# Kernel optimization log

Measured on AMD Instinct MI355X. Metric: run time of the kernel, lower is better.

Reference implementation:

```python
import jax, jax.numpy as jnp
import numpy as np

SHIFTS = [1, 2, 4]  # matches init_kwargs 'shifts' (all in range 0 < s < channels)


def setup_inputs() -> dict:
    key = jax.random.key(0)
    k1, k2, k3 = jax.random.split(key, 3)
    B, H, L, D = 4, 1, 2048, 512
    factor = 4
    proj_in = 2 * len(SHIFTS) * D  # cli_mode='full' -> 2 components per shift
    x = jax.random.normal(k1, (B, H, L, D), dtype=jnp.float32)
    W = jax.random.normal(k2, (factor, D), dtype=jnp.float32) * 0.05
    # glorot-ish scale for the projection kernel
    proj_kernel = jax.random.normal(k3, (proj_in, D), dtype=jnp.float32) * (1.0 / np.sqrt(proj_in))
    proj_bias = jnp.zeros((D,), dtype=jnp.float32)
    return {"x": x, "W": W, "proj_kernel": proj_kernel, "proj_bias": proj_bias}


def reference(x, W, proj_kernel, proj_bias):
    # x: (B, H, L, D); W: (k, D) slot multivectors
    k, D = W.shape
    B, H, L, _ = x.shape
    # coarse[-1] treated as zeros; non-anchor slots source previous coarse vector
    coarse_prev = jnp.pad(x, ((0, 0), (0, 0), (1, 0), (0, 0)))[:, :, :-1, :]
    # src: (B, H, L, k, D) — slots 0..k-2 from coarse_prev, slot k-1 (anchor) from x
    src = jnp.concatenate(
        [jnp.repeat(coarse_prev[:, :, :, None, :], k - 1, axis=3),
         x[:, :, :, None, :]],
        axis=3,
    )
    W_b = W[None, None, None, :, :]  # (1,1,1,k,D)
    components = []
    for s in SHIFTS:
        src_s = jnp.roll(src, s, axis=-1)
        W_s_b = jnp.roll(W, s, axis=-1)[None, None, None, :, :]
        sw = src * W_s_b
        components.append(sw - W_b * src_s)        # wedge part
        components.append(jax.nn.silu(sw))          # inner part (full mode)
    g = jnp.concatenate(components, axis=-1)  # (B,H,L,k, 2*len(shifts)*D)
    fine = jnp.einsum('bhlkc,cd->bhlkd', g, proj_kernel) + proj_bias
    return fine.reshape(B, H, L * k, D)
```

## Files before the change

### kernel.cpp

```cpp
#include <hip/hip_runtime.h>
#include <cstdint>
#include <cstddef>

#define D_DIM 512
#define L_DIM 2048
#define KB_DIM 2048
#define KS_DIM 1536
#define NROWS_X 2049
#define M_TOT 32768

typedef __bf16 bf16x8 __attribute__((ext_vector_type(8)));
typedef float  f32x4  __attribute__((ext_vector_type(4)));

__device__ __forceinline__ unsigned f2bf(float f) {
  unsigned u = __float_as_uint(f);
  u += 0x7FFF + ((u >> 16) & 1);
  return u >> 16;
}
__device__ __forceinline__ float bf2f(unsigned short u) {
  return __uint_as_float(((unsigned)u) << 16);
}
__device__ __forceinline__ void gld_lds16(const void* g, void* l) {
  __builtin_amdgcn_global_load_lds((const __attribute__((address_space(1))) void*)g,
                                   (__attribute__((address_space(3))) void*)l,
                                   16, 0, 0);
}

__global__ void convert_x(const float* __restrict__ x, unsigned short* __restrict__ XbfZ) {
  const int b = blockIdx.y;
  const int idx = blockIdx.x * 256 + threadIdx.x;
  if (idx >= NROWS_X * 128) return;
  const int rr = idx >> 7;
  const int c4 = idx & 127;
  uint2 p = {0u, 0u};
  if (rr > 0) {
    float4 v = reinterpret_cast<const float4*>(x)[((size_t)b * L_DIM + rr - 1) * 128 + c4];
    p.x = f2bf(v.x) | (f2bf(v.y) << 16);
    p.y = f2bf(v.z) | (f2bf(v.w) << 16);
  }
  reinterpret_cast<uint2*>(XbfZ)[((size_t)b * NROWS_X + rr) * 128 + c4] = p;
}

__global__ void build_B(const float* __restrict__ P, const float* __restrict__ W,
                        unsigned short* __restrict__ Ball,
                        unsigned short* __restrict__ Wtab, int buildWtab) {
  if (buildWtab && blockIdx.x == 0) {
    for (int i = threadIdx.x; i < 6144; i += 256) {
      const int c = i & 511; const int rest = i >> 9;
      const int si = rest % 3; const int jj = rest / 3;
      Wtab[(jj * 3 + si) * 512 + c] =
          (unsigned short)f2bf(W[jj * 512 + ((c - (1 << si)) & 511)]);
    }
  }
  const int bx = blockIdx.x;
  const int j = bx >> 6, dt = (bx >> 3) & 7, ct = bx & 7;
  const int t = threadIdx.x;
  const int d = dt * 64 + (t & 63);
  const int cbase = ct * 64 + (t >> 6) * 16;
  unsigned short bufd[16];
  unsigned short bufs[3][16];
  #pragma unroll
  for (int cc = 0; cc < 16; ++cc) {
    const int c = cbase + cc;
    float qd = 0.f;
    #pragma unroll
    for (int si = 0; si < 3; ++si) {
      const int s = 1 << si;
      const int cm = (c - s) & 511, cp = (c + s) & 511;
      qd += W[j * 512 + cm] * P[((size_t)(2 * si) * 512 + c) * 512 + d]
          - W[j * 512 + cp] * P[((size_t)(2 * si) * 512 + cp) * 512 + d];
      bufs[si][cc] = (unsigned short)f2bf(P[((size_t)(2 * si + 1) * 512 + c) * 512 + d]);
    }
    bufd[cc] = (unsigned short)f2bf(qd);
  }
  unsigned short* row = Ball + (size_t)(j * 512 + d) * KB_DIM;
  *reinterpret_cast<uint4*>(&row[cbase])     = *reinterpret_cast<uint4*>(&bufd[0]);
  *reinterpret_cast<uint4*>(&row[cbase + 8]) = *reinterpret_cast<uint4*>(&bufd[8]);
  #pragma unroll
  for (int si = 0; si < 3; ++si) {
    *reinterpret_cast<uint4*>(&row[512 + si * 512 + cbase])     = *reinterpret_cast<uint4*>(&bufs[si][0]);
    *reinterpret_cast<uint4*>(&row[512 + si * 512 + cbase + 8]) = *reinterpret_cast<uint4*>(&bufs[si][8]);
  }
}

__global__ void gs_gen(const unsigned short* __restrict__ XbfZ,
                       const unsigned short* __restrict__ Wtab,
                       unsigned short* __restrict__ GS) {
  const int m0 = blockIdx.x * 4;
  const int j = m0 >> 13, b = (m0 >> 11) & 3, lbase = m0 & 2047;
  const int r = threadIdx.x >> 6, lane = threadIdx.x & 63;
  const int l = lbase + r;
  const size_t vrow = (size_t)b * NROWS_X + l + (j == 3);
  union U { uint4 q; unsigned short s[8]; };
  U va;
  va.q = *reinterpret_cast<const uint4*>(XbfZ + vrow * 512 + lane * 8);
  unsigned short* o = GS + (size_t)(m0 + r) * KS_DIM + lane * 8;
  #pragma unroll
  for (int si = 0; si < 3; ++si) {
    U wa;
    wa.q = *reinterpret_cast<const uint4*>(Wtab + (j * 3 + si) * 512 + lane * 8);
    unsigned res[4];
    #pragma unroll
    for (int e = 0; e < 4; ++e) {
      float s0 = bf2f(va.s[2 * e])     * bf2f(wa.s[2 * e]);
      float s1 = bf2f(va.s[2 * e + 1]) * bf2f(wa.s[2 * e + 1]);
      float g0 = s0 * __builtin_amdgcn_rcpf(1.f + __expf(-s0));
      float g1 = s1 * __builtin_amdgcn_rcpf(1.f + __expf(-s1));
      res[e] = f2bf(g0) | (f2bf(g1) << 16);
    }
    uint4 ov = {res[0], res[1], res[2], res[3]};
    *reinterpret_cast<uint4*>(o + si * 512) = ov;
  }
}

#define BARR asm volatile("s_barrier" ::: "memory")
#define VMW(N) asm volatile("s_waitcnt vmcnt(" #N ")" ::: "memory")

#define READ_A(MH, BUF) do { \
  _Pragma("unroll") \
  for (int mf = 0; mf < 4; ++mf) { \
    a[mf][0] = __builtin_bit_cast(bf16x8, *reinterpret_cast<const uint4*>(&A_lds[BUF][aRow[mf] + (MH)*4096 + p0])); \
    a[mf][1] = __builtin_bit_cast(bf16x8, *reinterpret_cast<const uint4*>(&A_lds[BUF][aRow[mf] + (MH)*4096 + p1])); \
  } } while (0)

#define READ_B(NH, BUF, BB) do { \
  _Pragma("unroll") \
  for (int nf = 0; nf < 2; ++nf) { \
    BB[nf][0] = __builtin_bit_cast(bf16x8, *reinterpret_cast<const uint4*>(&B_lds[BUF][bRow[nf] + (NH)*2048 + p0])); \
    BB[nf][1] = __builtin_bit_cast(bf16x8, *reinterpret_cast<const uint4*>(&B_lds[BUF][bRow[nf] + (NH)*2048 + p1])); \
  } } while (0)

#define MFMA_Q(MH, NH, BB) do { \
  _Pragma("unroll") \
  for (int mf = 0; mf < 4; ++mf) { \
    _Pragma("unroll") \
    for (int nf = 0; nf < 2; ++nf) { \
      acc[(MH)*4+mf][(NH)*2+nf] = __builtin_amdgcn_mfma_f32_16x16x32_bf16(a[mf][0], BB[nf][0], acc[(MH)*4+mf][(NH)*2+nf], 0, 0, 0); \
      acc[(MH)*4+mf][(NH)*2+nf] = __builtin_amdgcn_mfma_f32_16x16x32_bf16(a[mf][1], BB[nf][1], acc[(MH)*4+mf][(NH)*2+nf], 0, 0, 0); \
    } } } while (0)

__global__ __launch_bounds__(512, 2) void gemm8(
    const unsigned short* __restrict__ XbfZ, const unsigned short* __restrict__ GS,
    const unsigned short* __restrict__ Ball, const float* __restrict__ bias,
    float* __restrict__ out) {
  __shared__ alignas(16) unsigned short A_lds[2][16384];
  __shared__ alignas(16) unsigned short B_lds[2][16384];

  const int tid = threadIdx.x;
  const int bid = blockIdx.x;
  const int wid = (bid & 7) * 32 + (bid >> 3);
  const int mtile = wid >> 1;
  const int ntile = wid & 1;
  const int j  = mtile >> 5;
  const int b  = (mtile >> 3) & 3;
  const int l0 = (mtile & 7) * 256;
  const int n0 = ntile * 256;
  const size_t mbase = (size_t)((j * 4 + b) * L_DIM + l0);

  const int srow = tid >> 3;
  const int c8   = (tid & 7) ^ (srow & 7);
  const unsigned short* pXd = XbfZ + ((size_t)(b * NROWS_X + (j == 3) + l0 + srow)) * 512 + c8 * 8;
  const unsigned short* pGS = GS + (mbase + srow) * (size_t)KS_DIM + c8 * 8;
  const unsigned short* pB  = Ball + ((size_t)(j * 512 + n0 + srow)) * KB_DIM + c8 * 8;
  const int ldsSlot = tid * 8;

  auto stageA = [&](int TT, int h, int bufi) {
    unsigned short* dst = &A_lds[bufi][h * 8192 + ldsSlot];
    if (TT < 8) {
      const unsigned short* s = pXd + (size_t)h * 128 * 512 + TT * 64;
      gld_lds16(s, dst);
      gld_lds16(s + 64 * 512, dst + 4096);
    } else {
      const unsigned short* s = pGS + (size_t)h * 128 * KS_DIM + (TT - 8) * 64;
      gld_lds16(s, dst);
      gld_lds16(s + 64 * KS_DIM, dst + 4096);
    }
  };
  auto stageB = [&](int TT, int h, int bufi) {
    const unsigned short* s = pB + (size_t)h * 128 * KB_DIM + TT * 64;
    unsigned short* dst = &B_lds[bufi][h * 8192 + ldsSlot];
    gld_lds16(s, dst);
    gld_lds16(s + 64 * KB_DIM, dst + 4096);
  };

  const int lane = tid & 63, wv = tid >> 6;
  const int wm = wv >> 2, wn = wv & 3;
  const int l16 = lane & 15, quad = lane >> 4;
  const int p0 = ((quad)     ^ (l16 & 7)) * 8;
  const int p1 = ((quad + 4) ^ (l16 & 7)) * 8;
  int aRow[4], bRow[2];
  #pragma unroll
  for (int mf = 0; mf < 4; ++mf) aRow[mf] = (wm * 128 + mf * 16 + l16) * 64;
  #pragma unroll
  for (int nf = 0; nf < 2; ++nf) bRow[nf] = (wn * 64 + nf * 16 + l16) * 64;

  f32x4 acc[8][4];
  #pragma unroll
  for (int i = 0; i < 8; ++i)
    #pragma unroll
    for (int n = 0; n < 4; ++n)
      acc[i][n] = f32x4{0.f, 0.f, 0.f, 0.f};

  bf16x8 a[4][2], b0[2][2], b1[2][2];

  stageB(0, 0, 0); stageB(0, 1, 0);
  stageA(0, 0, 0); stageA(0, 1, 0);
  stageB(1, 0, 1); stageB(1, 1, 1);
  VMW(4);
  BARR;

  for (int T = 0; T < 32; ++T) {
    const int cur = T & 1, nxt = cur ^ 1;
    READ_A(0, cur);
    READ_B(0, cur, b0);
    if (T + 1 < 32) stageA(T + 1, 0, nxt);
    BARR;
    __builtin_amdgcn_s_setprio(1);
    MFMA_Q(0, 0, b0);
    __builtin_amdgcn_s_setprio(0);
    BARR;
    READ_B(1, cur, b1);
    if (T + 1 < 32) stageA(T + 1, 1, nxt);
    BARR;
    __builtin_amdgcn_s_setprio(1);
    MFMA_Q(0, 1, b1);
    __builtin_amdgcn_s_setprio(0);
    BARR;
    READ_A(1, cur);
    if (T + 2 < 32) stageB(T + 2, 0, cur);
    BARR;
    __builtin_amdgcn_s_setprio(1);
    MFMA_Q(1, 1, b1);
    __builtin_amdgcn_s_setprio(0);
    BARR;
    if (T + 2 < 32) stageB(T + 2, 1, cur);
    BARR;
    __builtin_amdgcn_s_setprio(1);
    MFMA_Q(1, 0, b0);
    __builtin_amdgcn_s_setprio(0);
    if (T < 30) {
      VMW(4);
      BARR;
    } else if (T == 30) {
      VMW(0);
      BARR;
    }
  }

  #pragma unroll
  for (int nfg = 0; nfg < 4; ++nfg) {
    const int d = n0 + wn * 64 + nfg * 16 + l16;
    const float bv = bias[d];
    #pragma unroll
    for (int mfg = 0; mfg < 8; ++mfg) {
      const int lrow = l0 + wm * 128 + mfg * 16 + quad * 4;
      #pragma unroll
      for (int rg = 0; rg < 4; ++rg) {
        out[((size_t)(b * L_DIM + lrow + rg) * 4 + j) * D_DIM + d] = acc[mfg][nfg][rg] + bv;
      }
    }
  }
}

__global__ __launch_bounds__(256, 2) void fused_gemm(
    const unsigned short* __restrict__ XbfZ, const unsigned short* __restrict__ Ball,
    const float* __restrict__ W, const float* __restrict__ bias,
    float* __restrict__ out) {
  __shared__ alignas(16) unsigned short Vt[2][4096];
  __shared__ alignas(16) unsigned short Bt[2][8192];
  __shared__ alignas(16) unsigned short At[128 * 40];
  __shared__ alignas(16) unsigned short Wr[3 * 512];

  const int tid = threadIdx.x;
  const int nt = blockIdx.x & 1;
  const int mt = blockIdx.x >> 1;
  const int j  = mt >> 6;
  const int b  = (mt >> 4) & 3;
  const int lt = mt & 15;
  const int l0 = lt * 128;
  const int n0 = nt * 256;
  const int base_l = l0 - ((j == 3) ? 0 : 1);

  #pragma unroll
  for (int i = 0; i < 6; ++i) {
    const int idx = tid + i * 256;
    const int si = idx >> 9, c = idx & 511, s = 1 << si;
    Wr[idx] = (unsigned short)f2bf(W[j * 512 + ((c - s) & 511)]);
  }

  const int lane = tid & 63, wv = tid >> 6;
  const int qv = (lane & 3) ^ ((lane >> 4) & 3);
  const int rsub = lane >> 2;
  const unsigned short* gA0 = XbfZ + ((size_t)(b * NROWS_X + 1 + base_l + (wv * 2) * 16 + rsub)) * 512 + qv * 8;
  const unsigned short* gA1 = gA0 + (size_t)16 * 512;
  const unsigned short* gB[4];
  #pragma unroll
  for (int pi = 0; pi < 4; ++pi)
    gB[pi] = Ball + (size_t)(j * 512 + n0 + (wv * 4 + pi) * 16 + rsub) * KB_DIM + qv * 8;
  const int vOff0 = wv * 1024 + lane * 8;
  const int bOff0 = wv * 2048 + lane * 8;

  const int am = tid >> 1;
  const int akh = (tid & 1) * 16;
  const int ch0 = (tid & 1) * 2;
  const int sswz = (am >> 2) & 3;
  unsigned short* aDst = &At[am * 40 + akh];

  const int l16 = lane & 15, quad = lane >> 4;
  const int wm = wv >> 1, wn = wv & 1;
  const int fsw = (l16 >> 2) & 3;
  const int aVoff = (wm * 64 + l16) * 32 + ((quad ^ fsw)) * 8;
  const int aSoff = (wm * 64 + l16) * 40 + quad * 8;
  const int bOffF = (wn * 128 + l16) * 32 + ((quad ^ fsw)) * 8;

  f32x4 acc[4][8];
  #pragma unroll
  for (int i = 0; i < 4; ++i)
    #pragma unroll
    for (int n = 0; n < 8; ++n)
      acc[i][n] = f32x4{0.f, 0.f, 0.f, 0.f};

  {
    gld_lds16(gA0, &Vt[0][vOff0]);
    gld_lds16(gA1, &Vt[0][vOff0 + 512]);
    #pragma unroll
    for (int pi = 0; pi < 4; ++pi)
      gld_lds16(gB[pi], &Bt[0][bOff0 + pi * 512]);
  }

  for (int it = 0; it < 64; ++it) {
    const int buf = it & 1;
    const int kk0 = it * 32;
    const int gi = kk0 >> 9;

    __syncthreads();

    if (it + 1 < 64) {
      const int nk = kk0 + 32;
      const int nv = nk & 511;
      gld_lds16(gA0 + nv, &Vt[buf ^ 1][vOff0]);
      gld_lds16(gA1 + nv, &Vt[buf ^ 1][vOff0 + 512]);
      #pragma unroll
      for (int pi = 0; pi < 4; ++pi)
        gld_lds16(gB[pi] + nk, &Bt[buf ^ 1][bOff0 + pi * 512]);
    }

    bf16x8 af[4], bfr[8];
    if (gi == 0) {
      #pragma unroll
      for (int mi = 0; mi < 4; ++mi) {
        uint4 r = *reinterpret_cast<const uint4*>(&Vt[buf][aVoff + mi * 512]);
        af[mi] = __builtin_bit_cast(bf16x8, r);
      }
    } else {
      const int si = gi - 1;
      const int ccbase = (kk0 & 511) + akh;
      uint4 v0 = *reinterpret_cast<const uint4*>(&Vt[buf][(am * 4 + ((ch0)     ^ sswz)) * 8]);
      uint4 v1 = *reinterpret_cast<const uint4*>(&Vt[buf][(am * 4 + ((ch0 + 1) ^ sswz)) * 8]);
      uint4 w0 = *reinterpret_cast<const uint4*>(&Wr[si * 512 + ccbase]);
      uint4 w1 = *reinterpret_cast<const uint4*>(&Wr[si * 512 + ccbase + 8]);
      union U { uint4 q[2]; unsigned short s[16]; };
      U va, wa; va.q[0] = v0; va.q[1] = v1; wa.q[0] = w0; wa.q[1] = w1;
      unsigned res[8];
      #pragma unroll
      for (int e = 0; e < 8; ++e) {
        float s0 = bf2f(va.s[2 * e])     * bf2f(wa.s[2 * e]);
        float s1 = bf2f(va.s[2 * e + 1]) * bf2f(wa.s[2 * e + 1]);
        float g0 = s0 * __builtin_amdgcn_rcpf(1.f + __expf(-s0));
        float g1 = s1 * __builtin_amdgcn_rcpf(1.f + __expf(-s1));
        res[e] = f2bf(g0) | (f2bf(g1) << 16);
      }
      uint4 o0 = {res[0], res[1], res[2], res[3]};
      uint4 o1 = {res[4], res[5], res[6], res[7]};
      *reinterpret_cast<uint4*>(aDst) = o0;
      *reinterpret_cast<uint4*>(aDst + 8) = o1;
      __syncthreads();
      #pragma unroll
      for (int mi = 0; mi < 4; ++mi) {
        uint4 r = *reinterpret_cast<const uint4*>(&At[aSoff + mi * 640]);
        af[mi] = __builtin_bit_cast(bf16x8, r);
      }
    }
    #pragma unroll
    for (int ni = 0; ni < 8; ++ni) {
      uint4 r = *reinterpret_cast<const uint4*>(&Bt[buf][bOffF + ni * 512]);
      bfr[ni] = __builtin_bit_cast(bf16x8, r);
    }
    #pragma unroll
    for (int mi = 0; mi < 4; ++mi)
      #pragma unroll
      for (int ni = 0; ni < 8; ++ni)
        acc[mi][ni] = __builtin_amdgcn_mfma_f32_16x16x32_bf16(af[mi], bfr[ni], acc[mi][ni], 0, 0, 0);
  }

  #pragma unroll
  for (int ni = 0; ni < 8; ++ni) {
    const int d = n0 + wn * 128 + ni * 16 + l16;
    const float bv = bias[d];
    #pragma unroll
    for (int mi = 0; mi < 4; ++mi) {
      const int lrow = l0 + wm * 64 + mi * 16 + quad * 4;
      #pragma unroll
      for (int rg = 0; rg < 4; ++rg) {
        out[((size_t)(b * L_DIM + lrow + rg) * 4 + j) * D_DIM + d] = acc[mi][ni][rg] + bv;
      }
    }
  }
}

extern "C" void kernel_launch(void* const* d_in, const int* in_sizes, int n_in,
                              void* d_out, int out_size, void* d_ws, size_t ws_size,
                              hipStream_t stream) {
  const float* x    = (const float*)d_in[0];
  const float* W    = (const float*)d_in[1];
  const float* P    = (const float*)d_in[2];
  const float* bias = (const float*)d_in[3];
  float* out = (float*)d_out;

  unsigned short* XbfZ = (unsigned short*)d_ws;
  unsigned short* Ball = XbfZ + (size_t)4 * NROWS_X * 512;
  unsigned short* Wtab = Ball + (size_t)4 * 512 * KB_DIM;
  unsigned short* GS   = Wtab + 6144;
  const size_t need_bytes =
      ((size_t)4 * NROWS_X * 512 + (size_t)4 * 512 * KB_DIM + 6144 +
       (size_t)M_TOT * KS_DIM) * 2;
  const bool primary = ws_size >= need_bytes;

  convert_x<<<dim3(1025, 4), 256, 0, stream>>>(x, XbfZ);
  build_B<<<256, 256, 0, stream>>>(P, W, Ball, Wtab, primary ? 1 : 0);
  if (primary) {
    gs_gen<<<8192, 256, 0, stream>>>(XbfZ, Wtab, GS);
    gemm8<<<dim3(256), dim3(512), 0, stream>>>(XbfZ, GS, Ball, bias, out);
  } else {
    fused_gemm<<<512, 256, 0, stream>>>(XbfZ, Ball, W, bias, out);
  }
}
```

Measured before the change: 184.1 us.

## Switch main GEMM to 32x32x16 MFMA with two-phase K-step schedule

Replaces the 16x16x32 bf16 MFMA tiles in the primary GEMM with 32x32x16 MFMA tiles and 16-wide accumulators. Each K-step is restructured from four barrier-separated quarters into two halves, and both A halves are staged up front. The aim is fewer LDS fragment reads per FLOP, fewer barriers, and higher MFMA throughput per instruction. Risks include higher register pressure from the larger fragment arrays at 2 waves/SIMD, and a changed LDS read/write overlap that could race on buffer reuse.

```diff
diff --git a/kernel.cpp b/kernel.cpp
--- a/kernel.cpp
+++ b/kernel.cpp
@@ -11,6 +11,7 @@
 
 typedef __bf16 bf16x8 __attribute__((ext_vector_type(8)));
 typedef float  f32x4  __attribute__((ext_vector_type(4)));
+typedef float  f32x16 __attribute__((ext_vector_type(16)));
 
 __device__ __forceinline__ unsigned f2bf(float f) {
   unsigned u = __float_as_uint(f);
@@ -115,31 +116,9 @@
 
 #define BARR asm volatile("s_barrier" ::: "memory")
 #define VMW(N) asm volatile("s_waitcnt vmcnt(" #N ")" ::: "memory")
-
-#define READ_A(MH, BUF) do { \
-  _Pragma("unroll") \
-  for (int mf = 0; mf < 4; ++mf) { \
-    a[mf][0] = __builtin_bit_cast(bf16x8, *reinterpret_cast<const uint4*>(&A_lds[BUF][aRow[mf] + (MH)*4096 + p0])); \
-    a[mf][1] = __builtin_bit_cast(bf16x8, *reinterpret_cast<const uint4*>(&A_lds[BUF][aRow[mf] + (MH)*4096 + p1])); \
-  } } while (0)
-
-#define READ_B(NH, BUF, BB) do { \
-  _Pragma("unroll") \
-  for (int nf = 0; nf < 2; ++nf) { \
-    BB[nf][0] = __builtin_bit_cast(bf16x8, *reinterpret_cast<const uint4*>(&B_lds[BUF][bRow[nf] + (NH)*2048 + p0])); \
-    BB[nf][1] = __builtin_bit_cast(bf16x8, *reinterpret_cast<const uint4*>(&B_lds[BUF][bRow[nf] + (NH)*2048 + p1])); \
-  } } while (0)
-
-#define MFMA_Q(MH, NH, BB) do { \
-  _Pragma("unroll") \
-  for (int mf = 0; mf < 4; ++mf) { \
-    _Pragma("unroll") \
-    for (int nf = 0; nf < 2; ++nf) { \
-      acc[(MH)*4+mf][(NH)*2+nf] = __builtin_amdgcn_mfma_f32_16x16x32_bf16(a[mf][0], BB[nf][0], acc[(MH)*4+mf][(NH)*2+nf], 0, 0, 0); \
-      acc[(MH)*4+mf][(NH)*2+nf] = __builtin_amdgcn_mfma_f32_16x16x32_bf16(a[mf][1], BB[nf][1], acc[(MH)*4+mf][(NH)*2+nf], 0, 0, 0); \
-    } } } while (0)
-
-__global__ __launch_bounds__(512, 2) void gemm8(
+#define LDQ(BUFP, OFF) __builtin_bit_cast(bf16x8, *reinterpret_cast<const uint4*>(&(BUFP)[OFF]))
+
+__global__ __launch_bounds__(512, 2) void gemm32(
     const unsigned short* __restrict__ XbfZ, const unsigned short* __restrict__ GS,
     const unsigned short* __restrict__ Ball, const float* __restrict__ bias,
     float* __restrict__ out) {
@@ -185,23 +164,26 @@
 
   const int lane = tid & 63, wv = tid >> 6;
   const int wm = wv >> 2, wn = wv & 3;
-  const int l16 = lane & 15, quad = lane >> 4;
-  const int p0 = ((quad)     ^ (l16 & 7)) * 8;
-  const int p1 = ((quad + 4) ^ (l16 & 7)) * 8;
-  int aRow[4], bRow[2];
-  #pragma unroll
-  for (int mf = 0; mf < 4; ++mf) aRow[mf] = (wm * 128 + mf * 16 + l16) * 64;
-  #pragma unroll
-  for (int nf = 0; nf < 2; ++nf) bRow[nf] = (wn * 64 + nf * 16 + l16) * 64;
-
-  f32x4 acc[8][4];
-  #pragma unroll
-  for (int i = 0; i < 8; ++i)
-    #pragma unroll
-    for (int n = 0; n < 4; ++n)
-      acc[i][n] = f32x4{0.f, 0.f, 0.f, 0.f};
-
-  bf16x8 a[4][2], b0[2][2], b1[2][2];
+  const int l31 = lane & 31, hi = lane >> 5;
+  const int swz = l31 & 7;
+  int kpos[4];
+  #pragma unroll
+  for (int kc = 0; kc < 4; ++kc) kpos[kc] = (((kc * 2 + hi) ^ swz)) * 8;
+  const int aOff0 = (wm * 128 +  0 + l31) * 64;
+  const int aOff1 = (wm * 128 + 32 + l31) * 64;
+  const int aOff2 = (wm * 128 + 64 + l31) * 64;
+  const int aOff3 = (wm * 128 + 96 + l31) * 64;
+  const int bOff0 = (wn * 64 +  0 + l31) * 64;
+  const int bOff1 = (wn * 64 + 32 + l31) * 64;
+
+  f32x16 acc[4][2];
+  #pragma unroll
+  for (int i = 0; i < 4; ++i)
+    #pragma unroll
+    for (int n = 0; n < 2; ++n)
+      acc[i][n] = (f32x16)(0.f);
+
+  bf16x8 aF[2][4], bF[2][4];
 
   stageB(0, 0, 0); stageB(0, 1, 0);
   stageA(0, 0, 0); stageA(0, 1, 0);
@@ -211,32 +193,42 @@
 
   for (int T = 0; T < 32; ++T) {
     const int cur = T & 1, nxt = cur ^ 1;
-    READ_A(0, cur);
-    READ_B(0, cur, b0);
-    if (T + 1 < 32) stageA(T + 1, 0, nxt);
-    BARR;
+    const unsigned short* Ac = A_lds[cur];
+    const unsigned short* Bc = B_lds[cur];
+    if (T + 1 < 32) { stageA(T + 1, 0, nxt); stageA(T + 1, 1, nxt); }
+    #pragma unroll
+    for (int kc = 0; kc < 4; ++kc) {
+      const int kp = kpos[kc];
+      aF[0][kc] = LDQ(Ac, aOff0 + kp);
+      aF[1][kc] = LDQ(Ac, aOff1 + kp);
+      bF[0][kc] = LDQ(Bc, bOff0 + kp);
+      bF[1][kc] = LDQ(Bc, bOff1 + kp);
+    }
     __builtin_amdgcn_s_setprio(1);
-    MFMA_Q(0, 0, b0);
+    #pragma unroll
+    for (int kc = 0; kc < 4; ++kc) {
+      acc[0][0] = __builtin_amdgcn_mfma_f32_32x32x16_bf16(aF[0][kc], bF[0][kc], acc[0][0], 0, 0, 0);
+      acc[0][1] = __builtin_amdgcn_mfma_f32_32x32x16_bf16(aF[0][kc], bF[1][kc], acc[0][1], 0, 0, 0);
+      acc[1][0] = __builtin_amdgcn_mfma_f32_32x32x16_bf16(aF[1][kc], bF[0][kc], acc[1][0], 0, 0, 0);
+      acc[1][1] = __builtin_amdgcn_mfma_f32_32x32x16_bf16(aF[1][kc], bF[1][kc], acc[1][1], 0, 0, 0);
+    }
     __builtin_amdgcn_s_setprio(0);
-    BARR;
-    READ_B(1, cur, b1);
-    if (T + 1 < 32) stageA(T + 1, 1, nxt);
-    BARR;
+    if (T < 31) BARR;
+    if (T + 2 < 32) { stageB(T + 2, 0, cur); stageB(T + 2, 1, cur); }
+    #pragma unroll
+    for (int kc = 0; kc < 4; ++kc) {
+      const int kp = kpos[kc];
+      aF[0][kc] = LDQ(Ac, aOff2 + kp);
+      aF[1][kc] = LDQ(Ac, aOff3 + kp);
+    }
     __builtin_amdgcn_s_setprio(1);
-    MFMA_Q(0, 1, b1);
-    __builtin_amdgcn_s_setprio(0);
-    BARR;
-    READ_A(1, cur);
-    if (T + 2 < 32) stageB(T + 2, 0, cur);
-    BARR;
-    __builtin_amdgcn_s_setprio(1);
-    MFMA_Q(1, 1, b1);
-    __builtin_amdgcn_s_setprio(0);
-    BARR;
-    if (T + 2 < 32) stageB(T + 2, 1, cur);
-    BARR;
-    __builtin_amdgcn_s_setprio(1);
-    MFMA_Q(1, 0, b0);
+    #pragma unroll
+    for (int kc = 0; kc < 4; ++kc) {
+      acc[2][0] = __builtin_amdgcn_mfma_f32_32x32x16_bf16(aF[0][kc], bF[0][kc], acc[2][0], 0, 0, 0);
+      acc[2][1] = __builtin_amdgcn_mfma_f32_32x32x16_bf16(aF[0][kc], bF[1][kc], acc[2][1], 0, 0, 0);
+      acc[3][0] = __builtin_amdgcn_mfma_f32_32x32x16_bf16(aF[1][kc], bF[0][kc], acc[3][0], 0, 0, 0);
+      acc[3][1] = __builtin_amdgcn_mfma_f32_32x32x16_bf16(aF[1][kc], bF[1][kc], acc[3][1], 0, 0, 0);
+    }
     __builtin_amdgcn_s_setprio(0);
     if (T < 30) {
       VMW(4);
@@ -248,15 +240,16 @@
   }
 
   #pragma unroll
-  for (int nfg = 0; nfg < 4; ++nfg) {
-    const int d = n0 + wn * 64 + nfg * 16 + l16;
+  for (int nb = 0; nb < 2; ++nb) {
+    const int d = n0 + wn * 64 + nb * 32 + l31;
     const float bv = bias[d];
     #pragma unroll
-    for (int mfg = 0; mfg < 8; ++mfg) {
-      const int lrow = l0 + wm * 128 + mfg * 16 + quad * 4;
-      #pragma unroll
-      for (int rg = 0; rg < 4; ++rg) {
-        out[((size_t)(b * L_DIM + lrow + rg) * 4 + j) * D_DIM + d] = acc[mfg][nfg][rg] + bv;
+    for (int mb = 0; mb < 4; ++mb) {
+      const int rowbase = l0 + wm * 128 + mb * 32 + 4 * hi;
+      #pragma unroll
+      for (int rg = 0; rg < 16; ++rg) {
+        const int lrow = rowbase + (rg & 3) + 8 * (rg >> 2);
+        out[((size_t)(b * L_DIM + lrow) * 4 + j) * D_DIM + d] = acc[mb][nb][rg] + bv;
       }
     }
   }
@@ -430,7 +423,7 @@
   build_B<<<256, 256, 0, stream>>>(P, W, Ball, Wtab, primary ? 1 : 0);
   if (primary) {
     gs_gen<<<8192, 256, 0, stream>>>(XbfZ, Wtab, GS);
-    gemm8<<<dim3(256), dim3(512), 0, stream>>>(XbfZ, GS, Ball, bias, out);
+    gemm32<<<dim3(256), dim3(512), 0, stream>>>(XbfZ, GS, Ball, bias, out);
   } else {
     fused_gemm<<<512, 256, 0, stream>>>(XbfZ, Ball, W, bias, out);
   }
```

Measured after the change: 184.1 us. About the same (+0.0%).

## Fuse x conversion, B build and GS generation into one prep kernel; cut GEMM barriers

Applied to the files above, without the earlier changes.

Merges convert_x, build_B and gs_gen into a single prep launch. Each block converts one group of x rows to bf16 and directly emits the silu GS rows for all four slots from registers, using a per-block LDS copy of the W table instead of re-reading XbfZ from global memory. In the GEMM main loop, A and B staging is issued in larger batches and most intermediate barriers are dropped, which reduces synchronization but changes the order of LDS reads and global-to-LDS writes. Every prep block now rebuilds the W table, which adds redundant work, and the looser barrier scheme risks LDS read/write races.

```diff
diff --git a/kernel.cpp b/kernel.cpp
--- a/kernel.cpp
+++ b/kernel.cpp
@@ -26,37 +26,79 @@
                                    16, 0, 0);
 }
 
-__global__ void convert_x(const float* __restrict__ x, unsigned short* __restrict__ XbfZ) {
-  const int b = blockIdx.y;
-  const int idx = blockIdx.x * 256 + threadIdx.x;
-  if (idx >= NROWS_X * 128) return;
-  const int rr = idx >> 7;
-  const int c4 = idx & 127;
-  uint2 p = {0u, 0u};
-  if (rr > 0) {
-    float4 v = reinterpret_cast<const float4*>(x)[((size_t)b * L_DIM + rr - 1) * 128 + c4];
-    p.x = f2bf(v.x) | (f2bf(v.y) << 16);
-    p.y = f2bf(v.z) | (f2bf(v.w) << 16);
-  }
-  reinterpret_cast<uint2*>(XbfZ)[((size_t)b * NROWS_X + rr) * 128 + c4] = p;
-}
-
-__global__ void build_B(const float* __restrict__ P, const float* __restrict__ W,
-                        unsigned short* __restrict__ Ball,
-                        unsigned short* __restrict__ Wtab, int buildWtab) {
-  if (buildWtab && blockIdx.x == 0) {
-    for (int i = threadIdx.x; i < 6144; i += 256) {
+__global__ __launch_bounds__(256) void prep(
+    const float* __restrict__ x, const float* __restrict__ W, const float* __restrict__ P,
+    unsigned short* __restrict__ XbfZ, unsigned short* __restrict__ Ball,
+    unsigned short* __restrict__ GS, int doGS) {
+  __shared__ unsigned short WtabL[6144];
+  const int tid = threadIdx.x;
+
+  if (blockIdx.x < 2048) {
+    for (int i = tid; i < 6144; i += 256) {
       const int c = i & 511; const int rest = i >> 9;
       const int si = rest % 3; const int jj = rest / 3;
-      Wtab[(jj * 3 + si) * 512 + c] =
-          (unsigned short)f2bf(W[jj * 512 + ((c - (1 << si)) & 511)]);
-    }
-  }
-  const int bx = blockIdx.x;
+      WtabL[i] = (unsigned short)f2bf(W[jj * 512 + ((c - (1 << si)) & 511)]);
+    }
+    __syncthreads();
+
+    const int r = tid >> 6, lane = tid & 63;
+    const int gr = blockIdx.x * 4 + r;
+    const int b = gr >> 11, l = gr & 2047;
+
+    const float4* xr = reinterpret_cast<const float4*>(x) + ((size_t)(b * L_DIM + l)) * 128 + lane * 2;
+    const float4 v0 = xr[0], v1 = xr[1];
+    union U { uint4 q; unsigned short s[8]; };
+    U va;
+    va.q.x = f2bf(v0.x) | (f2bf(v0.y) << 16);
+    va.q.y = f2bf(v0.z) | (f2bf(v0.w) << 16);
+    va.q.z = f2bf(v1.x) | (f2bf(v1.y) << 16);
+    va.q.w = f2bf(v1.z) | (f2bf(v1.w) << 16);
+    *reinterpret_cast<uint4*>(XbfZ + ((size_t)(b * NROWS_X + l + 1)) * 512 + lane * 8) = va.q;
+
+    if (doGS) {
+      #pragma unroll
+      for (int j = 0; j < 4; ++j) {
+        const int lam = (j < 3) ? (l + 1) : l;
+        const bool wr = (j == 3) || (l < 2047);
+        unsigned short* o = GS + ((size_t)((j * 4 + b) * L_DIM + lam)) * KS_DIM + lane * 8;
+        #pragma unroll
+        for (int si = 0; si < 3; ++si) {
+          U wa;
+          wa.q = *reinterpret_cast<const uint4*>(&WtabL[(j * 3 + si) * 512 + lane * 8]);
+          unsigned res[4];
+          #pragma unroll
+          for (int e = 0; e < 4; ++e) {
+            float s0 = bf2f(va.s[2 * e])     * bf2f(wa.s[2 * e]);
+            float s1 = bf2f(va.s[2 * e + 1]) * bf2f(wa.s[2 * e + 1]);
+            float g0 = s0 * __builtin_amdgcn_rcpf(1.f + __expf(-s0));
+            float g1 = s1 * __builtin_amdgcn_rcpf(1.f + __expf(-s1));
+            res[e] = f2bf(g0) | (f2bf(g1) << 16);
+          }
+          if (wr) {
+            uint4 ov = {res[0], res[1], res[2], res[3]};
+            *reinterpret_cast<uint4*>(o + si * 512) = ov;
+          }
+        }
+      }
+    }
+    if (l == 2047) {
+      const uint4 z = {0u, 0u, 0u, 0u};
+      *reinterpret_cast<uint4*>(XbfZ + ((size_t)(b * NROWS_X)) * 512 + lane * 8) = z;
+      if (doGS) {
+        #pragma unroll
+        for (int j = 0; j < 3; ++j)
+          #pragma unroll
+          for (int si = 0; si < 3; ++si)
+            *reinterpret_cast<uint4*>(GS + ((size_t)((j * 4 + b) * L_DIM)) * KS_DIM + si * 512 + lane * 8) = z;
+      }
+    }
+    return;
+  }
+
+  const int bx = blockIdx.x - 2048;
   const int j = bx >> 6, dt = (bx >> 3) & 7, ct = bx & 7;
-  const int t = threadIdx.x;
-  const int d = dt * 64 + (t & 63);
-  const int cbase = ct * 64 + (t >> 6) * 16;
+  const int d = dt * 64 + (tid & 63);
+  const int cbase = ct * 64 + (tid >> 6) * 16;
   unsigned short bufd[16];
   unsigned short bufs[3][16];
   #pragma unroll
@@ -80,36 +122,6 @@
   for (int si = 0; si < 3; ++si) {
     *reinterpret_cast<uint4*>(&row[512 + si * 512 + cbase])     = *reinterpret_cast<uint4*>(&bufs[si][0]);
     *reinterpret_cast<uint4*>(&row[512 + si * 512 + cbase + 8]) = *reinterpret_cast<uint4*>(&bufs[si][8]);
-  }
-}
-
-__global__ void gs_gen(const unsigned short* __restrict__ XbfZ,
-                       const unsigned short* __restrict__ Wtab,
-                       unsigned short* __restrict__ GS) {
-  const int m0 = blockIdx.x * 4;
-  const int j = m0 >> 13, b = (m0 >> 11) & 3, lbase = m0 & 2047;
-  const int r = threadIdx.x >> 6, lane = threadIdx.x & 63;
-  const int l = lbase + r;
-  const size_t vrow = (size_t)b * NROWS_X + l + (j == 3);
-  union U { uint4 q; unsigned short s[8]; };
-  U va;
-  va.q = *reinterpret_cast<const uint4*>(XbfZ + vrow * 512 + lane * 8);
-  unsigned short* o = GS + (size_t)(m0 + r) * KS_DIM + lane * 8;
-  #pragma unroll
-  for (int si = 0; si < 3; ++si) {
-    U wa;
-    wa.q = *reinterpret_cast<const uint4*>(Wtab + (j * 3 + si) * 512 + lane * 8);
-    unsigned res[4];
-    #pragma unroll
-    for (int e = 0; e < 4; ++e) {
-      float s0 = bf2f(va.s[2 * e])     * bf2f(wa.s[2 * e]);
-      float s1 = bf2f(va.s[2 * e + 1]) * bf2f(wa.s[2 * e + 1]);
-      float g0 = s0 * __builtin_amdgcn_rcpf(1.f + __expf(-s0));
-      float g1 = s1 * __builtin_amdgcn_rcpf(1.f + __expf(-s1));
-      res[e] = f2bf(g0) | (f2bf(g1) << 16);
-    }
-    uint4 ov = {res[0], res[1], res[2], res[3]};
-    *reinterpret_cast<uint4*>(o + si * 512) = ov;
   }
 }
 
@@ -211,31 +223,19 @@
 
   for (int T = 0; T < 32; ++T) {
     const int cur = T & 1, nxt = cur ^ 1;
+    if (T + 1 < 32) { stageA(T + 1, 0, nxt); stageA(T + 1, 1, nxt); }
     READ_A(0, cur);
     READ_B(0, cur, b0);
-    if (T + 1 < 32) stageA(T + 1, 0, nxt);
-    BARR;
+    READ_B(1, cur, b1);
     __builtin_amdgcn_s_setprio(1);
     MFMA_Q(0, 0, b0);
-    __builtin_amdgcn_s_setprio(0);
-    BARR;
-    READ_B(1, cur, b1);
-    if (T + 1 < 32) stageA(T + 1, 1, nxt);
-    BARR;
-    __builtin_amdgcn_s_setprio(1);
     MFMA_Q(0, 1, b1);
     __builtin_amdgcn_s_setprio(0);
     BARR;
+    if (T + 2 < 32) { stageB(T + 2, 0, cur); stageB(T + 2, 1, cur); }
     READ_A(1, cur);
-    if (T + 2 < 32) stageB(T + 2, 0, cur);
-    BARR;
     __builtin_amdgcn_s_setprio(1);
     MFMA_Q(1, 1, b1);
-    __builtin_amdgcn_s_setprio(0);
-    BARR;
-    if (T + 2 < 32) stageB(T + 2, 1, cur);
-    BARR;
-    __builtin_amdgcn_s_setprio(1);
     MFMA_Q(1, 0, b0);
     __builtin_amdgcn_s_setprio(0);
     if (T < 30) {
@@ -419,17 +419,14 @@
 
   unsigned short* XbfZ = (unsigned short*)d_ws;
   unsigned short* Ball = XbfZ + (size_t)4 * NROWS_X * 512;
-  unsigned short* Wtab = Ball + (size_t)4 * 512 * KB_DIM;
-  unsigned short* GS   = Wtab + 6144;
+  unsigned short* GS   = Ball + (size_t)4 * 512 * KB_DIM + 6144;
   const size_t need_bytes =
       ((size_t)4 * NROWS_X * 512 + (size_t)4 * 512 * KB_DIM + 6144 +
        (size_t)M_TOT * KS_DIM) * 2;
   const bool primary = ws_size >= need_bytes;
 
-  convert_x<<<dim3(1025, 4), 256, 0, stream>>>(x, XbfZ);
-  build_B<<<256, 256, 0, stream>>>(P, W, Ball, Wtab, primary ? 1 : 0);
+  prep<<<2304, 256, 0, stream>>>(x, W, P, XbfZ, Ball, GS, primary ? 1 : 0);
   if (primary) {
-    gs_gen<<<8192, 256, 0, stream>>>(XbfZ, Wtab, GS);
     gemm8<<<dim3(256), dim3(512), 0, stream>>>(XbfZ, GS, Ball, bias, out);
   } else {
     fused_gemm<<<512, 256, 0, stream>>>(XbfZ, Ball, W, bias, out);
```

Result: faster. 175.5 us, median of 2 (-4.7%).
